# Kernel optimization log

Measured on AMD Instinct MI355X. Metric: run time of the kernel, lower is better.

## Reference

```python
import jax, jax.numpy as jnp
import numpy as np
from jax import lax

# channel-gather index lists for the 16 c3 branches (from the torch source)
IDX3 = np.array([0,1,2, 1,2,3, 2,3,4, 3,4,5, 0,4,5, 0,1,5])          # 6 branches x 3 ch
IDX4 = np.array([0,1,2,3, 1,2,3,4, 2,3,4,5, 0,3,4,5, 0,1,4,5,
                 0,1,2,5, 0,1,3,4, 1,2,4,5, 0,2,3,5])                  # 9 branches x 4 ch
F6_SCALE = 1.7519


def _conv(x, w, groups=1):
    # NCHW x OIHW, stride 1, VALID padding (all convs in the model)
    return lax.conv_general_dilated(x, w, (1, 1), 'VALID', feature_group_count=groups)


def _avgpool2(x):
    return lax.reduce_window(x, 0.0, lax.add, (1, 1, 2, 2), (1, 1, 2, 2), 'VALID') * 0.25


def _bconv(x, w, b, groups=1):
    # BinaryConvFunction.forward: sign(conv(sign(x), sign(w)) + b)
    out = _conv(jnp.sign(x), jnp.sign(w), groups) + b[None, :, None, None]
    return jnp.sign(out)


def setup_inputs() -> dict:
    key = jax.random.key(0)
    ks = jax.random.split(key, 16)
    B = 8192
    return {
        'x':     jax.random.normal(ks[0], (B, 1, 32, 32), jnp.float32),
        'c1_w':  jax.random.normal(ks[1], (6, 1, 5, 5), jnp.float32) * 0.2,
        'c1_b':  jax.random.normal(ks[2], (6,), jnp.float32) * 0.1,
        'w3':    jax.random.normal(ks[3], (6, 3, 5, 5), jnp.float32),   # 6 grouped 3-ch branches
        'b3':    jax.random.normal(ks[4], (6,), jnp.float32) * 0.1,
        'w4':    jax.random.normal(ks[5], (9, 4, 5, 5), jnp.float32),   # 9 grouped 4-ch branches
        'b4':    jax.random.normal(ks[6], (9,), jnp.float32) * 0.1,
        'w6':    jax.random.normal(ks[7], (1, 6, 5, 5), jnp.float32),   # 1 branch on all 6 ch
        'b6':    jax.random.normal(ks[8], (1,), jnp.float32) * 0.1,
        'c5_w':  jax.random.normal(ks[9], (120, 16, 5, 5), jnp.float32),
        'c5_b':  jax.random.normal(ks[10], (120,), jnp.float32) * 0.1,
        'f6_w':  jax.random.normal(ks[11], (84, 120), jnp.float32) * 0.1,
        'f6_b':  jax.random.normal(ks[12], (84,), jnp.float32) * 0.1,
        'rbf_w': jax.random.normal(ks[13], (10, 84), jnp.float32) * 0.1,
        'rbf_b': jax.random.normal(ks[14], (10,), jnp.float32) * 0.1,
    }


def reference(x, c1_w, c1_b, w3, b3, w4, b4, w6, b6, c5_w, c5_b, f6_w, f6_b, rbf_w, rbf_b):
    # c1 (full-precision conv) + relu + s2 avgpool: [B,1,32,32] -> [B,6,14,14]
    h = _avgpool2(jax.nn.relu(_conv(x, c1_w) + c1_b[None, :, None, None]))
    # 16 binary branch convs, batched as grouped convs over gathered channels
    o3 = _bconv(h[:, IDX3], w3, b3, groups=6)   # [B,6,10,10]
    o4 = _bconv(h[:, IDX4], w4, b4, groups=9)   # [B,9,10,10]
    o6 = _bconv(h, w6, b6)                      # [B,1,10,10]
    h = jnp.concatenate([o3, o4, o6], axis=1)   # [B,16,10,10] (matches torch cat order)
    h = _avgpool2(jax.nn.relu(h))               # [B,16,5,5]
    h = _bconv(h, c5_w, c5_b)                   # [B,120,1,1]
    h = h.reshape(h.shape[0], -1)               # [B,120]
    h = jnp.tanh((h @ f6_w.T + f6_b) * F6_SCALE)
    return jax.nn.relu(h @ rbf_w.T + rbf_b)     # [B,10]
```

## Files before the change

kernel.cpp:

```cpp
#include <hip/hip_runtime.h>
#include <stdint.h>

typedef float v2f __attribute__((ext_vector_type(2)));

#define NIMG 8

constexpr int IDX3[18] = {0,1,2, 1,2,3, 2,3,4, 3,4,5, 0,4,5, 0,1,5};
constexpr int IDX4[36] = {0,1,2,3, 1,2,3,4, 2,3,4,5, 0,3,4,5, 0,1,4,5,
                          0,1,2,5, 0,1,3,4, 1,2,4,5, 0,2,3,5};


__global__ void prepack_kernel(const float* __restrict__ w3, const float* __restrict__ w4,
                               const float* __restrict__ w6, const float* __restrict__ c5w,
                               unsigned* __restrict__ ws) {
    int t = blockIdx.x * blockDim.x + threadIdx.x;
    if (t < 60) {
        const float* src = (t < 18) ? (w3 + t * 25)
                          : (t < 54) ? (w4 + (t - 18) * 25)
                          : (w6 + (t - 54) * 25);
        unsigned m = 0;
        for (int p = 0; p < 25; ++p) if (src[p] > 0.f) m |= 1u << p;
        ws[t] = m;
    } else if (t < 1620) {
        int q = t - 60, oc = q / 13, w = q % 13;
        unsigned m = 0;
        for (int b = 0; b < 32; ++b) {
            int g = w * 32 + b;
            int qi = g >> 4, ic = g & 15;
            if (qi < 25 && c5w[oc * 400 + ic * 25 + qi] > 0.f) m |= 1u << b;
        }
        ws[60 + q] = m;
    }
}

__global__ __launch_bounds__(256, 4) void lenet_fused(
    const float* __restrict__ x, const float* __restrict__ c1w, const float* __restrict__ c1b,
    const float* __restrict__ b3, const float* __restrict__ b4, const float* __restrict__ b6,
    const float* __restrict__ c5b, const unsigned* __restrict__ ws,
    const float* __restrict__ f6w, const float* __restrict__ f6b,
    const float* __restrict__ rbfw, const float* __restrict__ rbfb,
    float* __restrict__ out, int B) {
    __shared__ float wS[150];
    __shared__ float bS[6], b3S[6], b4S[9], b6S[1];
    __shared__ unsigned hrow[NIMG][6][14];
    __shared__ unsigned sbits[NIMG][100];
    __shared__ unsigned c5in[NIMG][13];
    __shared__ float4 sS4[NIMG][30];
    __shared__ float f6o[NIMG][84];

    const int t = threadIdx.x;
    const int img0 = blockIdx.x * NIMG;
    const int nimg = min(NIMG, B - img0);

    if (t < 150) wS[t] = c1w[t];
    if (t < 6) { bS[t] = c1b[t]; b3S[t] = b3[t]; }
    if (t < 9) b4S[t] = b4[t];
    if (t == 0) b6S[0] = b6[0];
    __syncthreads();

    for (int q = t; q < nimg * 84; q += 256) {
        int py = q / (6 * NIMG), rem = q % (6 * NIMG), img = rem / 6, c = rem % 6;
        if (img >= nimg) continue;
        float wr[25];
        #pragma unroll
        for (int i = 0; i < 25; ++i) wr[i] = wS[c * 25 + i];
        const float bias = bS[c];
        v2f accp[28];
        #pragma unroll
        for (int j = 0; j < 28; ++j) accp[j] = (v2f){bias, bias};
        const float* xp = x + (size_t)(img0 + img) * 1024 + (2 * py) * 32;
        #pragma unroll
        for (int r = 0; r < 6; ++r) {
            float rv[32];
            #pragma unroll
            for (int q8 = 0; q8 < 8; ++q8) {
                float4 v = ((const float4*)(xp + r * 32))[q8];
                rv[4 * q8] = v.x; rv[4 * q8 + 1] = v.y; rv[4 * q8 + 2] = v.z; rv[4 * q8 + 3] = v.w;
            }
            if (r == 0) {
                #pragma unroll
                for (int kw = 0; kw < 5; ++kw) {
                    float wv = wr[kw];
                    #pragma unroll
                    for (int cx = 0; cx < 28; ++cx)
                        accp[cx].x = fmaf(rv[cx + kw], wv, accp[cx].x);
                }
            } else if (r == 5) {
                #pragma unroll
                for (int kw = 0; kw < 5; ++kw) {
                    float wv = wr[20 + kw];
                    #pragma unroll
                    for (int cx = 0; cx < 28; ++cx)
                        accp[cx].y = fmaf(rv[cx + kw], wv, accp[cx].y);
                }
            } else {
                v2f wp[5];
                #pragma unroll
                for (int kw = 0; kw < 5; ++kw)
                    wp[kw] = (v2f){wr[r * 5 + kw], wr[(r - 1) * 5 + kw]};
                #pragma unroll
                for (int kw = 0; kw < 5; ++kw) {
                    v2f w2 = wp[kw];
                    #pragma unroll
                    for (int cx = 0; cx < 28; ++cx) {
                        v2f x2 = (v2f){rv[cx + kw], rv[cx + kw]};
                        accp[cx] = x2 * w2 + accp[cx];
                    }
                }
            }
        }
        unsigned m = 0;
        #pragma unroll
        for (int px = 0; px < 14; ++px) {
            float mx = fmaxf(fmaxf(accp[2 * px].x, accp[2 * px].y),
                             fmaxf(accp[2 * px + 1].x, accp[2 * px + 1].y));
            if (mx > 0.f) m |= 1u << px;
        }
        hrow[img][c][py] = m;
    }
    __syncthreads();

    for (int q = t; q < nimg * 100; q += 256) {
        int img = q / 100, p = q % 100, oy = p / 10, ox = p % 10;
        unsigned win[6];
        int wpop[6];
        #pragma unroll
        for (int c = 0; c < 6; ++c) {
            unsigned w = 0;
            #pragma unroll
            for (int r = 0; r < 5; ++r)
                w |= ((hrow[img][c][oy + r] >> ox) & 31u) << (5 * r);
            win[c] = w;
            wpop[c] = __popc(w);
        }
        unsigned m16 = 0;
        #pragma unroll
        for (int br = 0; br < 6; ++br) {
            int sum = 0, tot = 0;
            #pragma unroll
            for (int j = 0; j < 3; ++j) {
                int c = IDX3[br * 3 + j];
                tot += wpop[c];
                sum += __popc(win[c] & ws[br * 3 + j]);
            }
            if ((float)(2 * sum - tot) + b3S[br] > 0.f) m16 |= 1u << br;
        }
        #pragma unroll
        for (int br = 0; br < 9; ++br) {
            int sum = 0, tot = 0;
            #pragma unroll
            for (int j = 0; j < 4; ++j) {
                int c = IDX4[br * 4 + j];
                tot += wpop[c];
                sum += __popc(win[c] & ws[18 + br * 4 + j]);
            }
            if ((float)(2 * sum - tot) + b4S[br] > 0.f) m16 |= 1u << (6 + br);
        }
        {
            int sum = 0, tot = 0;
            #pragma unroll
            for (int c = 0; c < 6; ++c) {
                tot += wpop[c];
                sum += __popc(win[c] & ws[54 + c]);
            }
            if ((float)(2 * sum - tot) + b6S[0] > 0.f) m16 |= 1u << 15;
        }
        sbits[img][p] = m16;
    }
    __syncthreads();

    for (int q = t; q < nimg * 13; q += 256) {
        int img = q / 13, j = q % 13;
        int qi0 = 2 * j;
        int qy = qi0 / 5, qx = qi0 % 5, base = 2 * qy * 10 + 2 * qx;
        unsigned a0 = sbits[img][base] | sbits[img][base + 1] |
                      sbits[img][base + 10] | sbits[img][base + 11];
        unsigned word = a0 & 0xFFFFu;
        if (j < 12) {
            int qi1 = qi0 + 1;
            qy = qi1 / 5; qx = qi1 % 5; base = 2 * qy * 10 + 2 * qx;
            unsigned a1 = sbits[img][base] | sbits[img][base + 1] |
                          sbits[img][base + 10] | sbits[img][base + 11];
            word |= (a1 & 0xFFFFu) << 16;
        }
        c5in[img][j] = word;
    }
    __syncthreads();

    for (int q = t; q < nimg * 120; q += 256) {
        int img = q / 120, oc = q % 120;
        const unsigned* cm = ws + 60 + oc * 13;
        int sum = 0, tot = 0;
        #pragma unroll
        for (int w = 0; w < 13; ++w) {
            unsigned inw = c5in[img][w];
            tot += __popc(inw);
            sum += __popc(inw & cm[w]);
        }
        bool pos = ((float)(2 * sum - tot) + c5b[oc]) > 0.f;
        ((float*)sS4)[img * 120 + oc] = pos ? 1.f : -1.f;
    }
    __syncthreads();

    for (int q = t; q < nimg * 84; q += 256) {
        int img = q / 84, j = q % 84;
        float acc = f6b[j];
        const float4* wrow = (const float4*)f6w + j * 30;
        #pragma unroll 6
        for (int kk = 0; kk < 30; ++kk) {
            float4 wv = wrow[kk];
            float4 sv = sS4[img][kk];
            acc = fmaf(sv.x, wv.x, acc);
            acc = fmaf(sv.y, wv.y, acc);
            acc = fmaf(sv.z, wv.z, acc);
            acc = fmaf(sv.w, wv.w, acc);
        }
        f6o[img][j] = tanhf(1.7519f * acc);
    }
    __syncthreads();

    if (t < nimg * 10) {
        int img = t / 10, oc = t % 10;
        float sum = rbfb[oc];
        const float4* rw = (const float4*)(rbfw + oc * 84);
        #pragma unroll
        for (int kk = 0; kk < 21; ++kk) {
            float4 wv = rw[kk];
            int j = 4 * kk;
            sum = fmaf(f6o[img][j + 0], wv.x, sum);
            sum = fmaf(f6o[img][j + 1], wv.y, sum);
            sum = fmaf(f6o[img][j + 2], wv.z, sum);
            sum = fmaf(f6o[img][j + 3], wv.w, sum);
        }
        out[(size_t)(img0 + img) * 10 + oc] = fmaxf(sum, 0.f);
    }
}

extern "C" void kernel_launch(void* const* d_in, const int* in_sizes, int n_in,
                              void* d_out, int out_size, void* d_ws, size_t ws_size,
                              hipStream_t stream) {
    const float* x    = (const float*)d_in[0];
    const float* c1w  = (const float*)d_in[1];
    const float* c1b  = (const float*)d_in[2];
    const float* w3   = (const float*)d_in[3];
    const float* b3   = (const float*)d_in[4];
    const float* w4   = (const float*)d_in[5];
    const float* b4   = (const float*)d_in[6];
    const float* w6   = (const float*)d_in[7];
    const float* b6   = (const float*)d_in[8];
    const float* c5w  = (const float*)d_in[9];
    const float* c5b  = (const float*)d_in[10];
    const float* f6w  = (const float*)d_in[11];
    const float* f6b  = (const float*)d_in[12];
    const float* rbfw = (const float*)d_in[13];
    const float* rbfb = (const float*)d_in[14];
    const int B = in_sizes[0] / 1024;

    unsigned* ws = (unsigned*)d_ws;

    prepack_kernel<<<dim3(7), dim3(256), 0, stream>>>(w3, w4, w6, c5w, ws);
    lenet_fused<<<dim3((B + NIMG - 1) / NIMG), dim3(256), 0, stream>>>(
        x, c1w, c1b, b3, b4, b6, c5b, ws, f6w, f6b, rbfw, rbfb, (float*)d_out, B);
}
```

Measured before the change: 164.2 us.

## Stage input images and c5 weight masks in LDS, cut images per block

Each block now copies its input images into padded shared memory (row stride 36 floats) with coalesced float4 loads, and the c1 conv reads rows from LDS rather than issuing repeated global loads. Work is remapped so each thread computes two pooled rows (py and py+7), keeping all threads busy with 6 images per block instead of 8. The c5 bit masks are also cached in shared memory. The larger LDS footprint lowers the occupancy hint to 2 blocks per SM and adds more blocks overall.

```diff
diff --git a/kernel.cpp b/kernel.cpp
--- a/kernel.cpp
+++ b/kernel.cpp
@@ -3,7 +3,7 @@
 
 typedef float v2f __attribute__((ext_vector_type(2)));
 
-#define NIMG 8
+#define NIMG 6
 
 constexpr int IDX3[18] = {0,1,2, 1,2,3, 2,3,4, 3,4,5, 0,4,5, 0,1,5};
 constexpr int IDX4[36] = {0,1,2,3, 1,2,3,4, 2,3,4,5, 0,3,4,5, 0,1,4,5,
@@ -33,15 +33,20 @@
     }
 }
 
-__global__ __launch_bounds__(256, 4) void lenet_fused(
+#define ROWS 36
+#define IMGS 1156
+
+__global__ __launch_bounds__(256, 2) void lenet_fused(
     const float* __restrict__ x, const float* __restrict__ c1w, const float* __restrict__ c1b,
     const float* __restrict__ b3, const float* __restrict__ b4, const float* __restrict__ b6,
     const float* __restrict__ c5b, const unsigned* __restrict__ ws,
     const float* __restrict__ f6w, const float* __restrict__ f6b,
     const float* __restrict__ rbfw, const float* __restrict__ rbfb,
     float* __restrict__ out, int B) {
+    __shared__ float xs[NIMG * IMGS];
     __shared__ float wS[150];
     __shared__ float bS[6], b3S[6], b4S[9], b6S[1];
+    __shared__ unsigned cmS[1560];
     __shared__ unsigned hrow[NIMG][6][14];
     __shared__ unsigned sbits[NIMG][100];
     __shared__ unsigned c5in[NIMG][13];
@@ -52,71 +57,84 @@
     const int img0 = blockIdx.x * NIMG;
     const int nimg = min(NIMG, B - img0);
 
+    {
+        const float4* src = (const float4*)(x + (size_t)img0 * 1024);
+        for (int i = t; i < nimg * 256; i += 256) {
+            int img = i >> 8, r = (i >> 3) & 31, q = i & 7;
+            ((float4*)xs)[img * 289 + r * 9 + q] = src[i];
+        }
+    }
+    for (int i = t; i < 1560; i += 256) cmS[i] = ws[60 + i];
     if (t < 150) wS[t] = c1w[t];
     if (t < 6) { bS[t] = c1b[t]; b3S[t] = b3[t]; }
     if (t < 9) b4S[t] = b4[t];
     if (t == 0) b6S[0] = b6[0];
     __syncthreads();
 
-    for (int q = t; q < nimg * 84; q += 256) {
-        int py = q / (6 * NIMG), rem = q % (6 * NIMG), img = rem / 6, c = rem % 6;
-        if (img >= nimg) continue;
+    if (t < nimg * 42) {
+        const int denom = nimg * 6;
+        int ph = t / denom, rem = t % denom, img = rem / 6, c = rem % 6;
         float wr[25];
         #pragma unroll
         for (int i = 0; i < 25; ++i) wr[i] = wS[c * 25 + i];
         const float bias = bS[c];
-        v2f accp[28];
-        #pragma unroll
-        for (int j = 0; j < 28; ++j) accp[j] = (v2f){bias, bias};
-        const float* xp = x + (size_t)(img0 + img) * 1024 + (2 * py) * 32;
-        #pragma unroll
-        for (int r = 0; r < 6; ++r) {
-            float rv[32];
-            #pragma unroll
-            for (int q8 = 0; q8 < 8; ++q8) {
-                float4 v = ((const float4*)(xp + r * 32))[q8];
-                rv[4 * q8] = v.x; rv[4 * q8 + 1] = v.y; rv[4 * q8 + 2] = v.z; rv[4 * q8 + 3] = v.w;
-            }
-            if (r == 0) {
+        #pragma unroll 1
+        for (int half = 0; half < 2; ++half) {
+            const int py = ph + 7 * half;
+            v2f accp[28];
+            #pragma unroll
+            for (int j = 0; j < 28; ++j) accp[j] = (v2f){bias, bias};
+            const float* xp = xs + img * IMGS + (2 * py) * ROWS;
+            #pragma unroll
+            for (int r = 0; r < 6; ++r) {
+                float rv[32];
                 #pragma unroll
-                for (int kw = 0; kw < 5; ++kw) {
-                    float wv = wr[kw];
-                    #pragma unroll
-                    for (int cx = 0; cx < 28; ++cx)
-                        accp[cx].x = fmaf(rv[cx + kw], wv, accp[cx].x);
+                for (int q8 = 0; q8 < 8; ++q8) {
+                    float4 v = ((const float4*)(xp + r * ROWS))[q8];
+                    rv[4 * q8] = v.x; rv[4 * q8 + 1] = v.y;
+                    rv[4 * q8 + 2] = v.z; rv[4 * q8 + 3] = v.w;
                 }
-            } else if (r == 5) {
-                #pragma unroll
-                for (int kw = 0; kw < 5; ++kw) {
-                    float wv = wr[20 + kw];
-                    #pragma unroll
-                    for (int cx = 0; cx < 28; ++cx)
-                        accp[cx].y = fmaf(rv[cx + kw], wv, accp[cx].y);
-                }
-            } else {
-                v2f wp[5];
-                #pragma unroll
-                for (int kw = 0; kw < 5; ++kw)
-                    wp[kw] = (v2f){wr[r * 5 + kw], wr[(r - 1) * 5 + kw]};
-                #pragma unroll
-                for (int kw = 0; kw < 5; ++kw) {
-                    v2f w2 = wp[kw];
-                    #pragma unroll
-                    for (int cx = 0; cx < 28; ++cx) {
-                        v2f x2 = (v2f){rv[cx + kw], rv[cx + kw]};
-                        accp[cx] = x2 * w2 + accp[cx];
+                if (r == 0) {
+                    #pragma unroll
+                    for (int kw = 0; kw < 5; ++kw) {
+                        float wv = wr[kw];
+                        #pragma unroll
+                        for (int cx = 0; cx < 28; ++cx)
+                            accp[cx].x = fmaf(rv[cx + kw], wv, accp[cx].x);
+                    }
+                } else if (r == 5) {
+                    #pragma unroll
+                    for (int kw = 0; kw < 5; ++kw) {
+                        float wv = wr[20 + kw];
+                        #pragma unroll
+                        for (int cx = 0; cx < 28; ++cx)
+                            accp[cx].y = fmaf(rv[cx + kw], wv, accp[cx].y);
+                    }
+                } else {
+                    v2f wp[5];
+                    #pragma unroll
+                    for (int kw = 0; kw < 5; ++kw)
+                        wp[kw] = (v2f){wr[r * 5 + kw], wr[(r - 1) * 5 + kw]};
+                    #pragma unroll
+                    for (int kw = 0; kw < 5; ++kw) {
+                        v2f w2 = wp[kw];
+                        #pragma unroll
+                        for (int cx = 0; cx < 28; ++cx) {
+                            v2f x2 = (v2f){rv[cx + kw], rv[cx + kw]};
+                            accp[cx] = x2 * w2 + accp[cx];
+                        }
                     }
                 }
             }
-        }
-        unsigned m = 0;
-        #pragma unroll
-        for (int px = 0; px < 14; ++px) {
-            float mx = fmaxf(fmaxf(accp[2 * px].x, accp[2 * px].y),
-                             fmaxf(accp[2 * px + 1].x, accp[2 * px + 1].y));
-            if (mx > 0.f) m |= 1u << px;
-        }
-        hrow[img][c][py] = m;
+            unsigned m = 0;
+            #pragma unroll
+            for (int px = 0; px < 14; ++px) {
+                float mx = fmaxf(fmaxf(accp[2 * px].x, accp[2 * px].y),
+                                 fmaxf(accp[2 * px + 1].x, accp[2 * px + 1].y));
+                if (mx > 0.f) m |= 1u << px;
+            }
+            hrow[img][c][py] = m;
+        }
     }
     __syncthreads();
 
@@ -169,8 +187,8 @@
     }
     __syncthreads();
 
-    for (int q = t; q < nimg * 13; q += 256) {
-        int img = q / 13, j = q % 13;
+    if (t < nimg * 13) {
+        int img = t / 13, j = t % 13;
         int qi0 = 2 * j;
         int qy = qi0 / 5, qx = qi0 % 5, base = 2 * qy * 10 + 2 * qx;
         unsigned a0 = sbits[img][base] | sbits[img][base + 1] |
@@ -189,7 +207,7 @@
 
     for (int q = t; q < nimg * 120; q += 256) {
         int img = q / 120, oc = q % 120;
-        const unsigned* cm = ws + 60 + oc * 13;
+        const unsigned* cm = cmS + oc * 13;
         int sum = 0, tot = 0;
         #pragma unroll
         for (int w = 0; w < 13; ++w) {
```

Measured after the change: 161.4 us. No clear change (-1.7%).
